# Kernel tuning notes

Measured on AMD Instinct MI355X. Metric: run time of the kernel, lower is better.

Reference implementation:

```python
import jax, jax.numpy as jnp
import numpy as np

N = 50000      # nodes
E = 640000     # edges
D_IN = 128     # input_dimension
H = 128        # hidden_dimension
D_OUT = 64     # output_dimension
G = 500        # num graphs
L = 2          # gnn layers (conv->norm->act stages each)
TEMP = 1.0     # mic_archi_param_temperature
EPS = 1e-5


def setup_inputs() -> dict:
    key = jax.random.key(0)
    ks = jax.random.split(key, 20)
    s = 1.0 / np.sqrt(H)
    inp = {
        "x": jax.random.normal(ks[0], (N, D_IN), jnp.float32),
        "edge_index": jax.random.randint(ks[1], (2, E), 0, N, dtype=jnp.int64),
        "batch": jnp.sort(jax.random.randint(ks[2], (N,), 0, G, dtype=jnp.int64)),
        # pre/post process MLPs (single Linear each)
        "pre_w": jax.random.normal(ks[3], (D_IN, H), jnp.float32) * s,
        "pre_b": jnp.zeros((H,), jnp.float32),
        "post_w": jax.random.normal(ks[4], (H, D_OUT), jnp.float32) * s,
        "post_b": jnp.zeros((D_OUT,), jnp.float32),
        # per-layer conv candidates: GCNConv + SAGEConv (stacked over L layers)
        "gcn_w": jax.random.normal(ks[5], (L, H, H), jnp.float32) * s,
        "gcn_b": jnp.zeros((L, H), jnp.float32),
        "sage_ws": jax.random.normal(ks[6], (L, H, H), jnp.float32) * s,
        "sage_wn": jax.random.normal(ks[7], (L, H, H), jnp.float32) * s,
        # per-layer norm candidate params (LayerNorm; Identity has none)
        "ln_g": jnp.ones((L, H), jnp.float32),
        "ln_b": jnp.zeros((L, H), jnp.float32),
        # architecture parameters (uniform init as in the torch code)
        "a_conv": jax.random.uniform(ks[8], (L, 2), jnp.float32),
        "a_norm": jax.random.uniform(ks[9], (L, 2), jnp.float32),
        "a_act": jax.random.uniform(ks[10], (L, 3), jnp.float32),
    }
    return inp


def reference(x, edge_index, batch, pre_w, pre_b, post_w, post_b,
              gcn_w, gcn_b, sage_ws, sage_wn, ln_g, ln_b,
              a_conv, a_norm, a_act):
    src, dst = edge_index[0], edge_index[1]
    loop = jnp.arange(N, dtype=src.dtype)
    # GCN uses self-loops + symmetric normalization
    src_sl = jnp.concatenate([src, loop])
    dst_sl = jnp.concatenate([dst, loop])
    deg = jax.ops.segment_sum(jnp.ones((E + N,), jnp.float32), dst_sl, num_segments=N)
    dinv = jax.lax.rsqrt(deg)  # deg >= 1 due to self-loops
    gcn_norm = (dinv[src_sl] * dinv[dst_sl])[:, None]  # [E+N, 1]
    # SAGE mean aggregation (no self loops)
    deg_n = jnp.clip(jax.ops.segment_sum(jnp.ones((E,), jnp.float32), dst, num_segments=N), 1.0)

    def gcn(h, w, b):
        hw = h @ w  # [N, H]
        agg = jax.ops.segment_sum(hw[src_sl] * gcn_norm, dst_sl, num_segments=N)
        return agg + b

    def sage(h, ws, wn):
        mean = jax.ops.segment_sum(h[src], dst, num_segments=N) / deg_n[:, None]
        return h @ ws + mean @ wn

    def layernorm(h, g, b):
        mu = jnp.mean(h, axis=-1, keepdims=True)
        var = jnp.mean(jnp.square(h - mu), axis=-1, keepdims=True)
        return (h - mu) * jax.lax.rsqrt(var + EPS) * g + b

    h = x @ pre_w + pre_b  # pre-process MLP
    layer_outputs = []
    for l in range(L):
        wc = jax.nn.softmax(a_conv[l] / TEMP)
        h = wc[0] * gcn(h, gcn_w[l], gcn_b[l]) + wc[1] * sage(h, sage_ws[l], sage_wn[l])
        wn_ = jax.nn.softmax(a_norm[l] / TEMP)
        h = wn_[0] * layernorm(h, ln_g[l], ln_b[l]) + wn_[1] * h
        wa = jax.nn.softmax(a_act[l] / TEMP)
        h = wa[0] * jax.nn.relu(h) + wa[1] * jnp.tanh(h) + wa[2] * jax.nn.elu(h)
        layer_outputs.append(h)  # collected after each act stage (skip connections)

    skip = layer_outputs[0]
    for o in layer_outputs[1:]:
        skip = skip + o
    pooled = jax.ops.segment_sum(skip, batch, num_segments=G)  # sum pooling readout
    return pooled @ post_w + post_b
```

## Files before the change

### kernel.cpp

```cpp
#include <hip/hip_runtime.h>
#include <hip/hip_fp16.h>
#include <math.h>

#define N_NODES 50000
#define N_EDGES 640000
#define HDIM    128
#define D_OUT   64
#define G_GRAPHS 500
#define EPSV    1e-5f
#define WPM     16384
#define CAP     64
#define SENT    N_NODES
#define NSHARD  8
#define SHARD_SZ ((N_NODES + NSHARD - 1) / NSHARD)

typedef __bf16 v8bf __attribute__((ext_vector_type(8)));
typedef float  f32x4 __attribute__((ext_vector_type(4)));

static __device__ __forceinline__ float bf_lo(unsigned u) {
    union { unsigned x; float f; } c; c.x = u << 16; return c.f;
}
static __device__ __forceinline__ float bf_hi(unsigned u) {
    union { unsigned x; float f; } c; c.x = u & 0xffff0000u; return c.f;
}

__global__ void setup_kernel(const float* __restrict__ pre_w,
                             const float* __restrict__ gcn_w,
                             const float* __restrict__ sws,
                             const float* __restrict__ swn,
                             const float* __restrict__ a_conv,
                             __bf16* __restrict__ Wp,
                             int* __restrict__ cnt,
                             float* __restrict__ pooled,
                             uint4* __restrict__ hrow0,
                             uint4* __restrict__ hrow1)
{
    int t = blockIdx.x * blockDim.x + threadIdx.x;
    if (t <= N_NODES) cnt[t] = 0;
    if (t < G_GRAPHS * 128) pooled[t] = 0.f;
    if (t < 16) {
        hrow0[t] = make_uint4(0, 0, 0, 0);
        hrow1[t] = make_uint4(0, 0, 0, 0);
    }
    if (t >= 7 * 2048) return;
    int m    = t >> 11;
    int r    = t & 2047;
    int lane = r & 63;
    int fb   = r >> 6;
    int kc   = fb >> 3;
    int cb   = fb & 7;
    const float* W = pre_w;
    float scale = 1.f;
    if (m > 0) {
        int type = (m - 1) >> 1;
        int l    = (m - 1) & 1;
        float c0 = a_conv[l * 2], c1 = a_conv[l * 2 + 1];
        float mx = fmaxf(c0, c1);
        float e0 = __expf(c0 - mx), e1 = __expf(c1 - mx);
        float wc0 = e0 / (e0 + e1);
        scale = (type == 0) ? wc0 : (1.f - wc0);
        W = (type == 0) ? gcn_w + (size_t)l * WPM
          : (type == 1) ? sws   + (size_t)l * WPM
                        : swn   + (size_t)l * WPM;
    }
    int k0  = kc * 32 + (lane >> 4) * 8;
    int col = cb * 16 + (lane & 15);
    __bf16* out = Wp + (size_t)m * WPM + ((size_t)fb * 64 + lane) * 8;
    #pragma unroll
    for (int i = 0; i < 8; i++)
        out[i] = (__bf16)(scale * W[(size_t)(k0 + i) * 128 + col]);
}

__global__ void csr_fill_kernel(const int* __restrict__ src, const int* __restrict__ dst,
                                int* __restrict__ cnt,
                                unsigned short* __restrict__ csr, int E) {
    int chunk = blockIdx.x >> 3;
    int shard = blockIdx.x & 7;
    int e = chunk * 256 + threadIdx.x;
    if (e >= E) return;
    int d = dst[e];
    if (d / SHARD_SZ != shard) return;
    int s = src[e];
    int pos = atomicAdd(&cnt[d], 1);
    csr[(d << 6) + pos] = (unsigned short)s;
}

__global__ __launch_bounds__(256) void fused_gather_bf16(
    const __bf16* __restrict__ hb,
    const unsigned short* __restrict__ csr,
    const int* __restrict__ cnt,
    __bf16* __restrict__ aggGb,
    __bf16* __restrict__ meanb, int n)
{
    int w = threadIdx.x >> 6;
    int lane = threadIdx.x & 63;
    int d = blockIdx.x * 4 + w;
    if (d >= n) return;
    int c = cnt[d];
    float cf = (float)c;
    float did = rsqrtf(cf + 1.0f);
    float rd  = 1.0f / fmaxf(cf, 1.0f);
    int base = d << 6;
    int full = c >> 4;
    int q  = lane >> 4;
    int c8 = (lane & 15) * 8;

    float aG[8] = {0, 0, 0, 0, 0, 0, 0, 0};
    float aS[8] = {0, 0, 0, 0, 0, 0, 0, 0};

    for (int p = 0; p < full; p++) {
        int s[4];
        #pragma unroll
        for (int k = 0; k < 4; k++)
            s[k] = csr[base + p * 16 + 4 * k + q];
        uint4 u[4];
        float ds[4];
        #pragma unroll
        for (int k = 0; k < 4; k++) {
            u[k]  = *(const uint4*)(hb + (size_t)s[k] * 128 + c8);
            ds[k] = rsqrtf((float)cnt[s[k]] + 1.0f);
        }
        #pragma unroll
        for (int k = 0; k < 4; k++) {
            float wk = ds[k] * did;
            float v[8] = { bf_lo(u[k].x), bf_hi(u[k].x), bf_lo(u[k].y), bf_hi(u[k].y),
                           bf_lo(u[k].z), bf_hi(u[k].z), bf_lo(u[k].w), bf_hi(u[k].w) };
            #pragma unroll
            for (int j = 0; j < 8; j++) {
                aG[j] = fmaf(v[j], wk, aG[j]);
                aS[j] += v[j];
            }
        }
    }
    if (c & 15) {
        int s[4];
        #pragma unroll
        for (int k = 0; k < 4; k++) {
            int idx = full * 16 + 4 * k + q;
            s[k] = (idx < c) ? (int)csr[base + idx] : SENT;
        }
        uint4 u[4];
        float ds[4];
        #pragma unroll
        for (int k = 0; k < 4; k++) {
            u[k]  = *(const uint4*)(hb + (size_t)s[k] * 128 + c8);
            ds[k] = rsqrtf((float)cnt[s[k]] + 1.0f);
        }
        #pragma unroll
        for (int k = 0; k < 4; k++) {
            float wk = ds[k] * did;
            float v[8] = { bf_lo(u[k].x), bf_hi(u[k].x), bf_lo(u[k].y), bf_hi(u[k].y),
                           bf_lo(u[k].z), bf_hi(u[k].z), bf_lo(u[k].w), bf_hi(u[k].w) };
            #pragma unroll
            for (int j = 0; j < 8; j++) {
                aG[j] = fmaf(v[j], wk, aG[j]);
                aS[j] += v[j];
            }
        }
    }
    #pragma unroll
    for (int j = 0; j < 8; j++) {
        aG[j] += __shfl_xor(aG[j], 16);
        aG[j] += __shfl_xor(aG[j], 32);
        aS[j] += __shfl_xor(aS[j], 16);
        aS[j] += __shfl_xor(aS[j], 32);
    }
    if (q == 0) {
        uint4 ud = *(const uint4*)(hb + (size_t)d * 128 + c8);
        float vd[8] = { bf_lo(ud.x), bf_hi(ud.x), bf_lo(ud.y), bf_hi(ud.y),
                        bf_lo(ud.z), bf_hi(ud.z), bf_lo(ud.w), bf_hi(ud.w) };
        float sl = did * did;
        union { __bf16 b[8]; uint4 u; } pg, pm;
        #pragma unroll
        for (int j = 0; j < 8; j++) {
            pg.b[j] = (__bf16)fmaf(vd[j], sl, aG[j]);
            pm.b[j] = (__bf16)(aS[j] * rd);
        }
        *(uint4*)(aggGb + (size_t)d * 128 + c8) = pg.u;
        *(uint4*)(meanb + (size_t)d * 128 + c8) = pm.u;
    }
}

__global__ __launch_bounds__(256) void pre_gemm_mfma(
    const float* __restrict__ x, const __bf16* __restrict__ Wp0,
    const float* __restrict__ pre_b, __bf16* __restrict__ hb, int n)
{
    __shared__ __bf16 wlds[WPM];
    const int tid  = threadIdx.x;
    const int w    = tid >> 6;
    const int lane = tid & 63;
    const int r0 = blockIdx.x * 64 + w * 16;
    int rl = r0 + (lane & 15);
    if (rl >= n) rl = n - 1;
    const int kg = lane >> 4;

    {
        uint4* lds4 = (uint4*)wlds;
        const uint4* g = (const uint4*)Wp0;
        #pragma unroll
        for (int it = 0; it < 8; it++)
            lds4[it * 256 + tid] = g[it * 256 + tid];
    }

    f32x4 acc[8];
    #pragma unroll
    for (int cb = 0; cb < 8; cb++) acc[cb] = (f32x4)(0.f);

    v8bf af[4];
    #pragma unroll
    for (int kc = 0; kc < 4; kc++) {
        const float* ap = x + (size_t)rl * 128 + kc * 32 + kg * 8;
        float4 a0 = *(const float4*)ap;
        float4 a1 = *(const float4*)(ap + 4);
        v8bf v;
        v[0] = (__bf16)a0.x; v[1] = (__bf16)a0.y;
        v[2] = (__bf16)a0.z; v[3] = (__bf16)a0.w;
        v[4] = (__bf16)a1.x; v[5] = (__bf16)a1.y;
        v[6] = (__bf16)a1.z; v[7] = (__bf16)a1.w;
        af[kc] = v;
    }
    __syncthreads();

    #pragma unroll
    for (int kc = 0; kc < 4; kc++) {
        #pragma unroll
        for (int cb = 0; cb < 8; cb++) {
            int bo = ((kc * 8 + cb) * 64 + lane) * 8;
            acc[cb] = __builtin_amdgcn_mfma_f32_16x16x32_bf16(
                af[kc], *(const v8bf*)&wlds[bo], acc[cb], 0, 0, 0);
        }
    }
    int cl = lane & 15;
    #pragma unroll
    for (int cb = 0; cb < 8; cb++) {
        float bias = pre_b[cb * 16 + cl];
        #pragma unroll
        for (int j = 0; j < 4; j++) {
            int r = r0 + kg * 4 + j;
            if (r < n) hb[(size_t)r * 128 + cb * 16 + cl] = (__bf16)(acc[cb][j] + bias);
        }
    }
}

__global__ __launch_bounds__(512, 4) void layer_gemm_kernel(
    const __bf16* __restrict__ aggGb, const __bf16* __restrict__ hin,
    const __bf16* __restrict__ meanb,
    const __bf16* __restrict__ WpG, const __bf16* __restrict__ WpS,
    const __bf16* __restrict__ WpN,
    const float* __restrict__ gcn_b,
    const float* __restrict__ lng, const float* __restrict__ lnb,
    const float* __restrict__ anorm, const float* __restrict__ aact,
    const float* __restrict__ aconv,
    __bf16* __restrict__ hout, int n)
{
    __shared__ __bf16 wlds[3 * 16 * 64 * 8];
    const int tid  = threadIdx.x;
    const int w    = tid >> 6;
    const int lane = tid & 63;
    const int r0 = blockIdx.x * 128 + w * 16;
    int rl = r0 + (lane & 15);
    if (rl >= n) rl = n - 1;
    const int kg = lane >> 4;

    v8bf af[12];
    #pragma unroll
    for (int kc = 0; kc < 4; kc++) {
        size_t ao = (size_t)rl * 128 + kc * 32 + kg * 8;
        af[kc]     = *(const v8bf*)(aggGb + ao);
        af[4 + kc] = *(const v8bf*)(hin   + ao);
        af[8 + kc] = *(const v8bf*)(meanb + ao);
    }

    f32x4 acc[8];
    #pragma unroll
    for (int cb = 0; cb < 8; cb++) acc[cb] = (f32x4)(0.f);

    uint4* lds4 = (uint4*)wlds;

    {
        const uint4* gG = (const uint4*)WpG;
        const uint4* gS = (const uint4*)WpS;
        const uint4* gN = (const uint4*)WpN;
        #pragma unroll
        for (int it = 0; it < 6; it++) {
            int idx = it * 512 + tid;
            int m = idx >> 10;
            int r = idx & 1023;
            const uint4* g = (m == 0) ? gG : (m == 1) ? gS : gN;
            lds4[idx] = g[r];
        }
    }
    __syncthreads();
    #pragma unroll
    for (int kc2 = 0; kc2 < 2; kc2++) {
        #pragma unroll
        for (int cb = 0; cb < 8; cb++) {
            int bo = ((kc2 * 8 + cb) * 64 + lane) * 8;
            acc[cb] = __builtin_amdgcn_mfma_f32_16x16x32_bf16(
                af[kc2], *(const v8bf*)&wlds[bo], acc[cb], 0, 0, 0);
            acc[cb] = __builtin_amdgcn_mfma_f32_16x16x32_bf16(
                af[4 + kc2], *(const v8bf*)&wlds[8192 + bo], acc[cb], 0, 0, 0);
            acc[cb] = __builtin_amdgcn_mfma_f32_16x16x32_bf16(
                af[8 + kc2], *(const v8bf*)&wlds[16384 + bo], acc[cb], 0, 0, 0);
        }
    }
    __syncthreads();

    {
        const uint4* gG = (const uint4*)WpG + 1024;
        const uint4* gS = (const uint4*)WpS + 1024;
        const uint4* gN = (const uint4*)WpN + 1024;
        #pragma unroll
        for (int it = 0; it < 6; it++) {
            int idx = it * 512 + tid;
            int m = idx >> 10;
            int r = idx & 1023;
            const uint4* g = (m == 0) ? gG : (m == 1) ? gS : gN;
            lds4[idx] = g[r];
        }
    }
    __syncthreads();
    #pragma unroll
    for (int kc2 = 0; kc2 < 2; kc2++) {
        #pragma unroll
        for (int cb = 0; cb < 8; cb++) {
            int bo = ((kc2 * 8 + cb) * 64 + lane) * 8;
            acc[cb] = __builtin_amdgcn_mfma_f32_16x16x32_bf16(
                af[2 + kc2], *(const v8bf*)&wlds[bo], acc[cb], 0, 0, 0);
            acc[cb] = __builtin_amdgcn_mfma_f32_16x16x32_bf16(
                af[6 + kc2], *(const v8bf*)&wlds[8192 + bo], acc[cb], 0, 0, 0);
            acc[cb] = __builtin_amdgcn_mfma_f32_16x16x32_bf16(
                af[10 + kc2], *(const v8bf*)&wlds[16384 + bo], acc[cb], 0, 0, 0);
        }
    }

    float c0 = aconv[0], c1 = aconv[1];
    float m = fmaxf(c0, c1);
    float e0 = __expf(c0 - m), e1 = __expf(c1 - m);
    float wc0 = e0 / (e0 + e1);
    float q0 = anorm[0], q1 = anorm[1];
    m = fmaxf(q0, q1);
    e0 = __expf(q0 - m); e1 = __expf(q1 - m);
    float wn0 = e0 / (e0 + e1), wn1 = 1.f - wn0;
    float a0 = aact[0], a1 = aact[1], a2 = aact[2];
    m = fmaxf(fmaxf(a0, a1), a2);
    float f0 = __expf(a0 - m), f1 = __expf(a1 - m), f2 = __expf(a2 - m);
    float fs = 1.f / (f0 + f1 + f2);
    float wa0 = f0 * fs, wa1 = f1 * fs, wa2 = f2 * fs;

    int cl = lane & 15;
    float gbF[8], lg[8], lb[8];
    #pragma unroll
    for (int cb = 0; cb < 8; cb++) {
        int c = cb * 16 + cl;
        gbF[cb] = wc0 * gcn_b[c]; lg[cb] = lng[c]; lb[cb] = lnb[c];
    }

    float s[4] = {0, 0, 0, 0}, s2[4] = {0, 0, 0, 0};
    #pragma unroll
    for (int cb = 0; cb < 8; cb++)
        #pragma unroll
        for (int j = 0; j < 4; j++) {
            float tv = acc[cb][j] + gbF[cb];
            acc[cb][j] = tv;
            s[j] += tv;
            s2[j] = fmaf(tv, tv, s2[j]);
        }
    #pragma unroll
    for (int o = 1; o < 16; o <<= 1)
        #pragma unroll
        for (int j = 0; j < 4; j++) {
            s[j]  += __shfl_xor(s[j], o);
            s2[j] += __shfl_xor(s2[j], o);
        }
    float mu[4], rs[4];
    #pragma unroll
    for (int j = 0; j < 4; j++) {
        mu[j] = s[j] * (1.f / 128.f);
        float var = s2[j] * (1.f / 128.f) - mu[j] * mu[j];
        rs[j] = rsqrtf(var + EPSV);
    }

    #pragma unroll
    for (int j = 0; j < 4; j++) {
        int r = r0 + kg * 4 + j;
        if (r >= n) continue;
        #pragma unroll
        for (int cb = 0; cb < 8; cb++) {
            float tv = acc[cb][j];
            float ln = (tv - mu[j]) * rs[j] * lg[cb] + lb[cb];
            float hv = wn0 * ln + wn1 * tv;
            float rl_ = fmaxf(hv, 0.f);
            float ex2 = __expf(2.f * hv);
            float th = 1.f - 2.f * __builtin_amdgcn_rcpf(ex2 + 1.f);
            float el = hv > 0.f ? hv : __expf(hv) - 1.f;
            float out = wa0 * rl_ + wa1 * th + wa2 * el;
            hout[(size_t)r * 128 + cb * 16 + cl] = (__bf16)out;
        }
    }
}

__global__ __launch_bounds__(256) void pool_sum_kernel(
    const __bf16* __restrict__ h1, const __bf16* __restrict__ h2,
    const int* __restrict__ batch, float* __restrict__ pooled, int n)
{
    int c2  = (threadIdx.x & 63) * 2;
    int seg = threadIdx.x >> 6;
    int n0  = blockIdx.x * 128 + seg * 32;
    int g_cur = -1;
    float acc0 = 0.f, acc1 = 0.f;
    for (int i = 0; i < 32; i++) {
        int node = n0 + i;
        if (node >= n) break;
        int g = batch[node];
        if (g != g_cur) {
            if (g_cur >= 0) {
                atomicAdd(&pooled[(size_t)g_cur * 128 + c2], acc0);
                atomicAdd(&pooled[(size_t)g_cur * 128 + c2 + 1], acc1);
            }
            g_cur = g; acc0 = 0.f; acc1 = 0.f;
        }
        unsigned u1 = *(const unsigned*)(h1 + (size_t)node * 128 + c2);
        unsigned u2 = *(const unsigned*)(h2 + (size_t)node * 128 + c2);
        acc0 += bf_lo(u1) + bf_lo(u2);
        acc1 += bf_hi(u1) + bf_hi(u2);
    }
    if (g_cur >= 0) {
        atomicAdd(&pooled[(size_t)g_cur * 128 + c2], acc0);
        atomicAdd(&pooled[(size_t)g_cur * 128 + c2 + 1], acc1);
    }
}

__global__ __launch_bounds__(64) void post_gemm_kernel(
    const float* __restrict__ pooled, const float* __restrict__ W,
    const float* __restrict__ b, float* __restrict__ out)
{
    __shared__ float p_s[128];
    int g = blockIdx.x;
    int j = threadIdx.x;
    p_s[j]      = pooled[(size_t)g * 128 + j];
    p_s[j + 64] = pooled[(size_t)g * 128 + 64 + j];
    __syncthreads();
    float acc = b[j];
    #pragma unroll
    for (int k = 0; k < 128; k++)
        acc = fmaf(p_s[k], W[k * 64 + j], acc);
    out[(size_t)g * 64 + j] = acc;
}

extern "C" void kernel_launch(void* const* d_in, const int* in_sizes, int n_in,
                              void* d_out, int out_size, void* d_ws, size_t ws_size,
                              hipStream_t stream)
{
    const float* x       = (const float*)d_in[0];
    const int*   ei      = (const int*)d_in[1];
    const int*   batch   = (const int*)d_in[2];
    const float* pre_w   = (const float*)d_in[3];
    const float* pre_b   = (const float*)d_in[4];
    const float* post_w  = (const float*)d_in[5];
    const float* post_b  = (const float*)d_in[6];
    const float* gcn_w   = (const float*)d_in[7];
    const float* gcn_b   = (const float*)d_in[8];
    const float* sage_ws = (const float*)d_in[9];
    const float* sage_wn = (const float*)d_in[10];
    const float* ln_g    = (const float*)d_in[11];
    const float* ln_b    = (const float*)d_in[12];
    const float* a_conv  = (const float*)d_in[13];
    const float* a_norm  = (const float*)d_in[14];
    const float* a_act   = (const float*)d_in[15];

    const int* src = ei;
    const int* dst = ei + N_EDGES;

    char* wsp = (char*)d_ws;
    size_t off = 0;
    auto alloc = [&](size_t bytes) {
        char* p = wsp + off;
        off += (bytes + 255) & ~(size_t)255;
        return p;
    };
    const size_t NHB = (size_t)(N_NODES + 1) * 128 * sizeof(__bf16);
    __bf16*         hb0    = (__bf16*)alloc(NHB);
    __bf16*         h1b    = (__bf16*)alloc(NHB);
    __bf16*         h2b    = (__bf16*)alloc(NHB);
    __bf16*         aggGb  = (__bf16*)alloc(NHB);
    __bf16*         meanb  = (__bf16*)alloc(NHB);
    __bf16*         Wp     = (__bf16*)alloc((size_t)7 * WPM * sizeof(__bf16));
    int*            cnt    = (int*)alloc((N_NODES + 1) * sizeof(int));
    unsigned short* csr    = (unsigned short*)alloc((size_t)N_NODES * CAP * sizeof(unsigned short));
    float*          pooled = (float*)alloc((size_t)G_GRAPHS * 128 * sizeof(float));

    const int PRE_BLOCKS   = (N_NODES + 63) / 64;
    const int LAYER_BLOCKS = (N_NODES + 127) / 128;
    const int GATHER_BLOCKS = (N_NODES + 3) / 4;
    const int SETUP_BLOCKS = (G_GRAPHS * 128 + 255) / 256;
    const int FILL_BLOCKS  = ((N_EDGES + 255) / 256) * NSHARD;

    setup_kernel<<<SETUP_BLOCKS, 256, 0, stream>>>(
        pre_w, gcn_w, sage_ws, sage_wn, a_conv, Wp, cnt, pooled,
        (uint4*)(hb0 + (size_t)N_NODES * 128),
        (uint4*)(h1b + (size_t)N_NODES * 128));

    csr_fill_kernel<<<FILL_BLOCKS, 256, 0, stream>>>(
        src, dst, cnt, csr, N_EDGES);

    pre_gemm_mfma<<<PRE_BLOCKS, 256, 0, stream>>>(x, Wp, pre_b, hb0, N_NODES);

    const __bf16* hin[2]  = { hb0, h1b };
    __bf16*       hout[2] = { h1b, h2b };
    for (int l = 0; l < 2; l++) {
        fused_gather_bf16<<<GATHER_BLOCKS, 256, 0, stream>>>(
            hin[l], csr, cnt, aggGb, meanb, N_NODES);
        layer_gemm_kernel<<<LAYER_BLOCKS, 512, 0, stream>>>(
            aggGb, hin[l], meanb,
            Wp + (size_t)(1 + l) * WPM, Wp + (size_t)(3 + l) * WPM, Wp + (size_t)(5 + l) * WPM,
            gcn_b + l * 128, ln_g + l * 128, ln_b + l * 128,
            a_norm + l * 2, a_act + l * 3, a_conv + l * 2,
            hout[l], N_NODES);
    }

    pool_sum_kernel<<<(N_NODES + 127) / 128, 256, 0, stream>>>(h1b, h2b, batch, pooled, N_NODES);
    post_gemm_kernel<<<G_GRAPHS, 64, 0, stream>>>(pooled, post_w, post_b, (float*)d_out);
}
```

Baseline: 176.9 us.

## Fuse pooling readout and post GEMM into one per-graph kernel

Replaces the atomic-based sum pooling kernel and the separate post GEMM kernel with a single kernel that runs one block per graph. Each block finds its node range by binary search on the sorted batch array, reduces across four waves in shared memory, and applies the output linear layer. This drops the zeroing of the pooled buffer, the float atomics and one kernel launch. It relies on batch being sorted, and each block walks its roughly 100 nodes serially across only four waves.

Result: faster. 169.2 us (-4.3%).

```diff
diff --git a/kernel.cpp b/kernel.cpp
--- a/kernel.cpp
+++ b/kernel.cpp
@@ -31,13 +31,11 @@
                              const float* __restrict__ a_conv,
                              __bf16* __restrict__ Wp,
                              int* __restrict__ cnt,
-                             float* __restrict__ pooled,
                              uint4* __restrict__ hrow0,
                              uint4* __restrict__ hrow1)
 {
     int t = blockIdx.x * blockDim.x + threadIdx.x;
     if (t <= N_NODES) cnt[t] = 0;
-    if (t < G_GRAPHS * 128) pooled[t] = 0.f;
     if (t < 16) {
         hrow0[t] = make_uint4(0, 0, 0, 0);
         hrow1[t] = make_uint4(0, 0, 0, 0);
@@ -400,52 +398,45 @@
     }
 }
 
-__global__ __launch_bounds__(256) void pool_sum_kernel(
+__global__ __launch_bounds__(256) void pool_post_kernel(
     const __bf16* __restrict__ h1, const __bf16* __restrict__ h2,
-    const int* __restrict__ batch, float* __restrict__ pooled, int n)
+    const int* __restrict__ batch,
+    const float* __restrict__ W, const float* __restrict__ b,
+    float* __restrict__ out, int n)
 {
-    int c2  = (threadIdx.x & 63) * 2;
-    int seg = threadIdx.x >> 6;
-    int n0  = blockIdx.x * 128 + seg * 32;
-    int g_cur = -1;
-    float acc0 = 0.f, acc1 = 0.f;
-    for (int i = 0; i < 32; i++) {
-        int node = n0 + i;
-        if (node >= n) break;
-        int g = batch[node];
-        if (g != g_cur) {
-            if (g_cur >= 0) {
-                atomicAdd(&pooled[(size_t)g_cur * 128 + c2], acc0);
-                atomicAdd(&pooled[(size_t)g_cur * 128 + c2 + 1], acc1);
-            }
-            g_cur = g; acc0 = 0.f; acc1 = 0.f;
-        }
-        unsigned u1 = *(const unsigned*)(h1 + (size_t)node * 128 + c2);
-        unsigned u2 = *(const unsigned*)(h2 + (size_t)node * 128 + c2);
-        acc0 += bf_lo(u1) + bf_lo(u2);
-        acc1 += bf_hi(u1) + bf_hi(u2);
-    }
-    if (g_cur >= 0) {
-        atomicAdd(&pooled[(size_t)g_cur * 128 + c2], acc0);
-        atomicAdd(&pooled[(size_t)g_cur * 128 + c2 + 1], acc1);
-    }
-}
-
-__global__ __launch_bounds__(64) void post_gemm_kernel(
-    const float* __restrict__ pooled, const float* __restrict__ W,
-    const float* __restrict__ b, float* __restrict__ out)
-{
-    __shared__ float p_s[128];
-    int g = blockIdx.x;
-    int j = threadIdx.x;
-    p_s[j]      = pooled[(size_t)g * 128 + j];
-    p_s[j + 64] = pooled[(size_t)g * 128 + 64 + j];
+    __shared__ float ps[4][128];
+    __shared__ float pool_s[128];
+    const int g   = blockIdx.x;
+    const int tid = threadIdx.x;
+    const int wv  = tid >> 6;
+    const int lane = tid & 63;
+
+    int lo = 0, hi = n;
+    while (lo < hi) { int mid = (lo + hi) >> 1; if (batch[mid] < g) lo = mid + 1; else hi = mid; }
+    int beg = lo;
+    hi = n;
+    while (lo < hi) { int mid = (lo + hi) >> 1; if (batch[mid] < g + 1) lo = mid + 1; else hi = mid; }
+    int end = lo;
+
+    float a0 = 0.f, a1 = 0.f;
+    for (int node = beg + wv; node < end; node += 4) {
+        unsigned u1 = *(const unsigned*)(h1 + (size_t)node * 128 + lane * 2);
+        unsigned u2 = *(const unsigned*)(h2 + (size_t)node * 128 + lane * 2);
+        a0 += bf_lo(u1) + bf_lo(u2);
+        a1 += bf_hi(u1) + bf_hi(u2);
+    }
+    ps[wv][lane * 2]     = a0;
+    ps[wv][lane * 2 + 1] = a1;
     __syncthreads();
-    float acc = b[j];
-    #pragma unroll
-    for (int k = 0; k < 128; k++)
-        acc = fmaf(p_s[k], W[k * 64 + j], acc);
-    out[(size_t)g * 64 + j] = acc;
+    if (tid < 128) pool_s[tid] = ps[0][tid] + ps[1][tid] + ps[2][tid] + ps[3][tid];
+    __syncthreads();
+    if (tid < 64) {
+        float acc = b[tid];
+        #pragma unroll
+        for (int k = 0; k < 128; k++)
+            acc = fmaf(pool_s[k], W[k * 64 + tid], acc);
+        out[(size_t)g * 64 + tid] = acc;
+    }
 }
 
 extern "C" void kernel_launch(void* const* d_in, const int* in_sizes, int n_in,
@@ -488,16 +479,15 @@
     __bf16*         Wp     = (__bf16*)alloc((size_t)7 * WPM * sizeof(__bf16));
     int*            cnt    = (int*)alloc((N_NODES + 1) * sizeof(int));
     unsigned short* csr    = (unsigned short*)alloc((size_t)N_NODES * CAP * sizeof(unsigned short));
-    float*          pooled = (float*)alloc((size_t)G_GRAPHS * 128 * sizeof(float));
-
-    const int PRE_BLOCKS   = (N_NODES + 63) / 64;
-    const int LAYER_BLOCKS = (N_NODES + 127) / 128;
+
+    const int PRE_BLOCKS    = (N_NODES + 63) / 64;
+    const int LAYER_BLOCKS  = (N_NODES + 127) / 128;
     const int GATHER_BLOCKS = (N_NODES + 3) / 4;
-    const int SETUP_BLOCKS = (G_GRAPHS * 128 + 255) / 256;
-    const int FILL_BLOCKS  = ((N_EDGES + 255) / 256) * NSHARD;
+    const int SETUP_BLOCKS  = (N_NODES + 1 + 255) / 256;
+    const int FILL_BLOCKS   = ((N_EDGES + 255) / 256) * NSHARD;
 
     setup_kernel<<<SETUP_BLOCKS, 256, 0, stream>>>(
-        pre_w, gcn_w, sage_ws, sage_wn, a_conv, Wp, cnt, pooled,
+        pre_w, gcn_w, sage_ws, sage_wn, a_conv, Wp, cnt,
         (uint4*)(hb0 + (size_t)N_NODES * 128),
         (uint4*)(h1b + (size_t)N_NODES * 128));
 
@@ -519,6 +509,6 @@
             hout[l], N_NODES);
     }
 
-    pool_sum_kernel<<<(N_NODES + 127) / 128, 256, 0, stream>>>(h1b, h2b, batch, pooled, N_NODES);
-    post_gemm_kernel<<<G_GRAPHS, 64, 0, stream>>>(pooled, post_w, post_b, (float*)d_out);
-}
+    pool_post_kernel<<<G_GRAPHS, 256, 0, stream>>>(
+        h1b, h2b, batch, post_w, post_b, (float*)d_out, N_NODES);
+}
```
